# Kernel tuning notes

Measured on AMD Instinct MI355X. Metric: run time of the kernel, lower is better.

The kernel has to match this reference:

```python
import jax, jax.numpy as jnp
import numpy as np

B, N = 32, 128
V, P, L = 50000, 40, 50
WD, UD = 100, 25
D = WD + UD          # 125: LSTM hidden per direction
H2 = 2 * D           # 250: BiLSTM output
HID = 100            # hidden_dim for scorers


def setup_inputs() -> dict:
    key = jax.random.key(0)
    ks = iter(jax.random.split(key, 40))
    p = lambda shape: jax.random.normal(next(ks), shape, jnp.float32) * 0.05
    inp = {
        'word_ids': jax.random.randint(next(ks), (B, N), 0, V),
        'upos_ids': jax.random.randint(next(ks), (B, N), 0, P),
        'target_arcs': jax.random.randint(next(ks), (B, N), 0, N),
        'wlookup': p((V, WD)),
        'tlookup': p((V, UD)),  # original sizes tag table by word_count
        # LSTM layer 0 (input D=125), layer 1 (input 2D=250); f=fwd, b=bwd dir
        'l0f_Wih': p((4 * D, D)), 'l0f_Whh': p((4 * D, D)), 'l0f_b': p((4 * D,)),
        'l0b_Wih': p((4 * D, D)), 'l0b_Whh': p((4 * D, D)), 'l0b_b': p((4 * D,)),
        'l1f_Wih': p((4 * D, H2)), 'l1f_Whh': p((4 * D, D)), 'l1f_b': p((4 * D,)),
        'l1b_Wih': p((4 * D, H2)), 'l1b_Whh': p((4 * D, D)), 'l1b_b': p((4 * D,)),
        'eh_W': p((HID, H2)), 'eh_b': p((HID,)),
        'em_W': p((HID, H2)), 'em_b': p((HID,)),
        'es_W': p((1, HID)), 'es_b': p((1,)),
        'lh_W': p((HID, H2)), 'lh_b': p((HID,)),
        'lm_W': p((HID, H2)), 'lm_b': p((HID,)),
        'ls_W': p((L, HID)), 'ls_b': p((L,)),
    }
    return inp


def _lstm_dir(x, Wih, Whh, b, reverse):
    # x: [B,T,in] -> h: [B,T,H], pytorch gate order i,f,g,o
    H = Whh.shape[1]
    xg = jnp.einsum('bti,gi->btg', x, Wih) + b  # precompute input projections

    def step(carry, xt):
        h, c = carry
        g = xt + h @ Whh.T
        i, f, gg, o = jnp.split(g, 4, axis=-1)
        c = jax.nn.sigmoid(f) * c + jax.nn.sigmoid(i) * jnp.tanh(gg)
        h = jax.nn.sigmoid(o) * jnp.tanh(c)
        return (h, c), h

    h0 = jnp.zeros((x.shape[0], H), x.dtype)
    _, hs = jax.lax.scan(step, (h0, h0), jnp.swapaxes(xg, 0, 1), reverse=reverse)
    return jnp.swapaxes(hs, 0, 1)


def _bilstm(x, Wf, Uf, bf, Wb, Ub, bb):
    return jnp.concatenate([_lstm_dir(x, Wf, Uf, bf, False),
                            _lstm_dir(x, Wb, Ub, bb, True)], axis=-1)


def reference(word_ids, upos_ids, target_arcs, wlookup, tlookup,
              l0f_Wih, l0f_Whh, l0f_b, l0b_Wih, l0b_Whh, l0b_b,
              l1f_Wih, l1f_Whh, l1f_b, l1b_Wih, l1b_Whh, l1b_b,
              eh_W, eh_b, em_W, em_b, es_W, es_b,
              lh_W, lh_b, lm_W, lm_b, ls_W, ls_b):
    n = word_ids.shape[1]
    words = jnp.concatenate([wlookup[word_ids], tlookup[upos_ids]], axis=-1)  # [B,N,125]
    h0 = _bilstm(words, l0f_Wih, l0f_Whh, l0f_b, l0b_Wih, l0b_Whh, l0b_b)
    word_exprs = _bilstm(h0, l1f_Wih, l1f_Whh, l1f_b, l1b_Wih, l1b_Whh, l1b_b)  # [B,N,250]

    word_h = word_exprs @ eh_W.T + eh_b  # [B,N,100]
    word_m = word_exprs @ em_W.T + em_b
    # fused pairwise biaffine-style scoring (replaces the O(n) python loop)
    pair = jnp.tanh(word_h[:, :, None, :] + word_m[:, None, :, :])  # [B,N,N,100]
    arc_scores = jnp.einsum('bijh,h->bij', pair, es_W[0]) + es_b[0]  # [B,N,N]

    # training path: margin augmentation
    target_arcs = target_arcs.at[:, 0].set(0)
    margin = 1.0 - jax.nn.one_hot(target_arcs, n, dtype=arc_scores.dtype)
    arc_scores = arc_scores + margin

    # decode() is an external MST decoder; greedy argmax stand-in
    parsed_trees = jnp.argmax(arc_scores, axis=-1)

    tree = target_arcs  # is_train path
    rel_heads = jnp.take_along_axis(word_exprs, tree[:, :, None], axis=1)  # [B,N,250]
    rel_heads = rel_heads @ lh_W.T + lh_b
    rel_mod = word_exprs @ lm_W.T + lm_b
    rel_scores = jnp.tanh(rel_mod + rel_heads) @ ls_W.T + ls_b  # [B,N,L]
    predicted_rels = jnp.argmax(rel_scores, axis=-1)
    return (parsed_trees, predicted_rels, arc_scores, rel_scores)
```

## Files before the change

kernel.cpp:

```cpp
#include <hip/hip_runtime.h>
#include <hip/hip_bf16.h>
#include <hip/hip_fp16.h>
#include <math.h>

#define B 32
#define N 128
#define BT (B*N)
#define WD 100
#define UD 25
#define D 125
#define G4 (4*D)
#define H2 (2*D)
#define HID 100
#define L 50

__device__ __forceinline__ float fast_tanh(float x) {
    float e = __expf(2.0f * x);
    return 1.0f - 2.0f / (e + 1.0f);
}
__device__ __forceinline__ float fast_sigmoid(float x) {
    return 1.0f / (1.0f + __expf(-x));
}
__device__ __forceinline__ float bcast_lane(float v, int k) {
    return __builtin_bit_cast(float, __builtin_amdgcn_readlane(__builtin_bit_cast(int, v), k));
}
__device__ __forceinline__ unsigned bcast_lane_u(unsigned v, int k) {
    return (unsigned)__builtin_amdgcn_readlane((int)v, k);
}

__device__ __forceinline__ unsigned pack_f16x2(float lo, float hi) {
    __half hl = __float2half_rn(lo), hh = __float2half_rn(hi);
    unsigned a = (unsigned)__builtin_bit_cast(unsigned short, hl);
    unsigned b = (unsigned)__builtin_bit_cast(unsigned short, hh);
    return a | (b << 16);
}

typedef _Float16 h2_t __attribute__((ext_vector_type(2)));
__device__ __forceinline__ float dot2acc(unsigned wu, unsigned hu, float acc) {
#if __has_builtin(__builtin_amdgcn_fdot2)
    return __builtin_amdgcn_fdot2(__builtin_bit_cast(h2_t, wu),
                                  __builtin_bit_cast(h2_t, hu), acc, false);
#else
    h2_t wv = __builtin_bit_cast(h2_t, wu);
    h2_t hv = __builtin_bit_cast(h2_t, hu);
    acc = fmaf((float)wv[0], (float)hv[0], acc);
    acc = fmaf((float)wv[1], (float)hv[1], acc);
    return acc;
#endif
}

struct TJob { const float* src; float* dst; int R, C, ldo, coff, tile0, tiles_x; };
struct TArgs { TJob j[8]; };

__global__ __launch_bounds__(256)
void setup_fused(TArgs a, int n_tr,
                 const int* __restrict__ wids, const int* __restrict__ uids,
                 const float* __restrict__ wl, const float* __restrict__ tl,
                 float* __restrict__ words,
                 const float* __restrict__ l0f_b, const float* __restrict__ l0b_b,
                 const float* __restrict__ l1f_b, const float* __restrict__ l1b_b,
                 const float* __restrict__ eh_b, const float* __restrict__ em_b,
                 const float* __restrict__ lm_b,
                 float* __restrict__ b_l0, float* __restrict__ b_l1,
                 float* __restrict__ b_s3,
                 const float* __restrict__ s0, const float* __restrict__ s1,
                 const float* __restrict__ s2, const float* __restrict__ s3w,
                 unsigned* __restrict__ d0, unsigned* __restrict__ d1,
                 unsigned* __restrict__ d2, unsigned* __restrict__ d3) {
    __shared__ float tile[32][33];
    int bid = blockIdx.x;
    int tid = threadIdx.x;
    if (bid < n_tr) {
        int ji = 0;
        #pragma unroll
        for (int i = 1; i < 8; i++) if (bid >= a.j[i].tile0) ji = i;
        TJob jb = a.j[ji];
        int t = bid - jb.tile0;
        int tx = t % jb.tiles_x, ty = t / jb.tiles_x;
        int txx = tid & 31, tyy = tid >> 5;
        int k0 = tx*32, n0 = ty*32;
        #pragma unroll
        for (int dy = 0; dy < 32; dy += 8) {
            int n = n0 + tyy + dy, k = k0 + txx;
            if (n < jb.R && k < jb.C)
                tile[tyy+dy][txx] = jb.src[(size_t)n*jb.C + k];
        }
        __syncthreads();
        #pragma unroll
        for (int dy = 0; dy < 32; dy += 8) {
            int k = k0 + tyy + dy, n = n0 + txx;
            if (k < jb.C && n < jb.R)
                jb.dst[(size_t)k*jb.ldo + jb.coff + n] = tile[txx][tyy+dy];
        }
        return;
    }
    bid -= n_tr;
    if (bid < 2048) {
        int bt = bid*2 + (tid >> 7);
        int t = tid & 127;
        int wid = wids[bt], uid = uids[bt];
        if (t < WD)       words[bt*D + t] = wl[(size_t)wid*WD + t];
        else if (t < D)   words[bt*D + t] = tl[(size_t)uid*UD + (t - WD)];
        return;
    }
    bid -= 2048;
    if (bid < 9) {
        int t = bid*256 + tid;
        if (t < 500)        b_l0[t] = l0f_b[t];
        else if (t < 1000)  b_l0[t] = l0b_b[t-500];
        else if (t < 1500)  b_l1[t-1000] = l1f_b[t-1000];
        else if (t < 2000)  b_l1[t-1000] = l1b_b[t-1500];
        else if (t < 2100)  b_s3[t-2000] = eh_b[t-2000];
        else if (t < 2200)  b_s3[t-2000] = em_b[t-2100];
        else if (t < 2300)  b_s3[t-2000] = lm_b[t-2200];
        return;
    }
    bid -= 9;
    int e = bid*256 + tid;
    int m = e >> 15;
    int r = e & 32767;
    int pk = r >> 9;
    int g  = r & 511;
    const float* s = (m == 0) ? s0 : (m == 1) ? s1 : (m == 2) ? s2 : s3w;
    unsigned* dd   = (m == 0) ? d0 : (m == 1) ? d1 : (m == 2) ? d2 : d3;
    float v0 = 0.0f, v1 = 0.0f;
    if (g < 500) {
        int k0 = pk << 1;
        if (k0 < 125)     v0 = s[(size_t)g*125 + k0];
        if (k0 + 1 < 125) v1 = s[(size_t)g*125 + k0 + 1];
    }
    dd[(pk << 9) + g] = pack_f16x2(v0, v1);
}

#define MT 16
template<int CPT, int BD>
__device__ __forceinline__
void proj_body(const float* __restrict__ x, const float* __restrict__ WT,
               const float* __restrict__ bias, float* __restrict__ out,
               int Ncols, int K, int ldx, const int* __restrict__ gather_idx,
               int blk, float* xs) {
    int m0 = blk * MT;
    for (int e = threadIdx.x; e < MT * K; e += BD) {
        int r = e / K, k = e - r * K;
        int m = m0 + r;
        int row = m;
        if (gather_idx) {
            int bb = m >> 7, np = m & 127;
            row = (bb << 7) + (np == 0 ? 0 : gather_idx[m]);
        }
        xs[k*17 + r] = x[(size_t)row*ldx + k];
    }
    __syncthreads();
    int n0 = threadIdx.x;
    int lane = threadIdx.x & 63;
    float acc[CPT][MT];
    int ncl[CPT];
    #pragma unroll
    for (int j = 0; j < CPT; j++) {
        int n = n0 + j*BD;
        ncl[j] = (n < Ncols) ? n : (Ncols - 1);
        #pragma unroll
        for (int r = 0; r < MT; r++) acc[j][r] = 0.0f;
    }
    float wkc[4][CPT];
    #pragma unroll
    for (int q = 0; q < 4; q++)
        #pragma unroll
        for (int j = 0; j < CPT; j++)
            wkc[q][j] = WT[(size_t)q*Ncols + ncl[j]];
    int k0 = 0;
    for (; k0 + 8 <= K; k0 += 4) {
        float xv = xs[(k0 + (lane >> 4))*17 + (lane & 15)];
        float wkn[4][CPT];
        #pragma unroll
        for (int q = 0; q < 4; q++)
            #pragma unroll
            for (int j = 0; j < CPT; j++)
                wkn[q][j] = WT[(size_t)(k0 + 4 + q)*Ncols + ncl[j]];
        #pragma unroll
        for (int q = 0; q < 4; q++) {
            #pragma unroll
            for (int r = 0; r < 16; r++) {
                float hv = bcast_lane(xv, q*16 + r);
                #pragma unroll
                for (int j = 0; j < CPT; j++)
                    acc[j][r] = fmaf(wkc[q][j], hv, acc[j][r]);
            }
        }
        #pragma unroll
        for (int q = 0; q < 4; q++)
            #pragma unroll
            for (int j = 0; j < CPT; j++)
                wkc[q][j] = wkn[q][j];
    }
    {
        float xv = xs[(k0 + (lane >> 4))*17 + (lane & 15)];
        #pragma unroll
        for (int q = 0; q < 4; q++) {
            #pragma unroll
            for (int r = 0; r < 16; r++) {
                float hv = bcast_lane(xv, q*16 + r);
                #pragma unroll
                for (int j = 0; j < CPT; j++)
                    acc[j][r] = fmaf(wkc[q][j], hv, acc[j][r]);
            }
        }
        k0 += 4;
    }
    for (; k0 < K; k0++) {
        float xv = xs[k0*17 + (lane & 15)];
        float wk[CPT];
        #pragma unroll
        for (int j = 0; j < CPT; j++) wk[j] = WT[(size_t)k0*Ncols + ncl[j]];
        #pragma unroll
        for (int r = 0; r < 16; r++) {
            float hv = bcast_lane(xv, r);
            #pragma unroll
            for (int j = 0; j < CPT; j++)
                acc[j][r] = fmaf(wk[j], hv, acc[j][r]);
        }
    }
    #pragma unroll
    for (int j = 0; j < CPT; j++) {
        int n = n0 + j*BD;
        if (n < Ncols) {
            float bb = bias[n];
            #pragma unroll
            for (int r = 0; r < MT; r++) out[(size_t)(m0 + r)*Ncols + n] = acc[j][r] + bb;
        }
    }
}

__global__ __launch_bounds__(512)
void proj_t(const float* __restrict__ x, const float* __restrict__ WT,
            const float* __restrict__ bias, float* __restrict__ out,
            int Ncols, int K, int ldx) {
    __shared__ float xs[250 * 17 + 16];
    proj_body<2, 512>(x, WT, bias, out, Ncols, K, ldx, nullptr, blockIdx.x, xs);
}

__global__ __launch_bounds__(256)
void proj_s3lh(const float* __restrict__ x,
               const float* __restrict__ WTa, const float* __restrict__ ba,
               float* __restrict__ outa,
               const float* __restrict__ WTb, const float* __restrict__ bb,
               float* __restrict__ outb, const int* __restrict__ gather_idx) {
    __shared__ float xs[250 * 17 + 16];
    int job = blockIdx.x >> 8;
    int blk = blockIdx.x & 255;
    if (job == 0)
        proj_body<2, 256>(x, WTa, ba, outa, 300, H2, H2, nullptr, blk, xs);
    else
        proj_body<2, 256>(x, WTb, bb, outb, 100, H2, H2, gather_idx, blk, xs);
}

__global__ __launch_bounds__(512, 2)
void lstm_scan(const float* __restrict__ xgc,
               const unsigned* __restrict__ WhHf, const unsigned* __restrict__ WhHb,
               float* __restrict__ out) {
    int dir = blockIdx.x & 1;
    int b = blockIdx.x >> 1;
    const unsigned* WhH = dir ? WhHb : WhHf;
    int off = dir ? D : 0;
    int t = threadIdx.x;
    int lane = t & 63;
    int w = t >> 6;
    int ks = w >> 1;
    int cg = ((w & 1) << 6) + lane;
    int c0 = cg << 2;

    __shared__ __align__(16) float hbuf[128];
    __shared__ __align__(16) float pbuf[4*512];

    const unsigned* wp = WhH + (size_t)(ks*16)*512 + c0;

    const float* xb = xgc + (size_t)b * N * 1000 + dir * 500;
    bool xa = (ks == 0) && (cg < 125);
    float4 zero4 = make_float4(0.f, 0.f, 0.f, 0.f);
    float4 xA = zero4, xB = zero4;
    if (xa) {
        xA = *(const float4*)&xb[(size_t)(dir ? (N-1) : 0)*1000 + c0];
        xB = *(const float4*)&xb[(size_t)(dir ? (N-2) : 1)*1000 + c0];
    }

    if (t < 128) hbuf[t] = 0.0f;
    __syncthreads();

    float c = 0.0f;
    for (int ti = 0; ti < N; ti++) {
        int tt = dir ? (N-1-ti) : ti;
        uint4 wq[16];
        #pragma unroll
        for (int p = 0; p < 16; p++)
            wq[p] = *(const uint4*)&wp[(size_t)p*512];
        float2 h2 = *(const float2*)&hbuf[ks*32 + ((lane & 15) << 1)];
        unsigned vhp = pack_f16x2(h2.x, h2.y);
        float4 x_cur = xA;
        float4 xC = zero4;
        if (xa && ti + 2 < N) {
            int tn = dir ? (tt-2) : (tt+2);
            xC = *(const float4*)&xb[(size_t)tn*1000 + c0];
        }
        float a0 = x_cur.x, a1 = x_cur.y, a2 = x_cur.z, a3 = x_cur.w;
        #pragma unroll
        for (int p = 0; p < 16; p++) {
            unsigned hp = bcast_lane_u(vhp, p);
            a0 = dot2acc(wq[p].x, hp, a0);
            a1 = dot2acc(wq[p].y, hp, a1);
            a2 = dot2acc(wq[p].z, hp, a2);
            a3 = dot2acc(wq[p].w, hp, a3);
        }
        xA = xB; xB = xC;
        *(float4*)&pbuf[ks*512 + c0] = make_float4(a0, a1, a2, a3);
        asm volatile("s_waitcnt lgkmcnt(0)" ::: "memory");
        __builtin_amdgcn_s_barrier();
        asm volatile("" ::: "memory");
        if (t < D) {
            float iv = pbuf[t]       + pbuf[512+t]       + pbuf[1024+t]       + pbuf[1536+t];
            float fv = pbuf[125+t]   + pbuf[512+125+t]   + pbuf[1024+125+t]   + pbuf[1536+125+t];
            float gv = pbuf[250+t]   + pbuf[512+250+t]   + pbuf[1024+250+t]   + pbuf[1536+250+t];
            float ov = pbuf[375+t]   + pbuf[512+375+t]   + pbuf[1024+375+t]   + pbuf[1536+375+t];
            float si = fast_sigmoid(iv);
            float sf = fast_sigmoid(fv);
            float so = fast_sigmoid(ov);
            c = sf * c + si * fast_tanh(gv);
            float h = so * fast_tanh(c);
            hbuf[t] = h;
            out[(size_t)(b*N + tt)*H2 + off + t] = h;
        }
        asm volatile("s_waitcnt lgkmcnt(0)" ::: "memory");
        __builtin_amdgcn_s_barrier();
        asm volatile("" ::: "memory");
    }
}

#define ITILE 4
__global__ __launch_bounds__(128)
void arc_rel(const float* __restrict__ s3,
             const float* __restrict__ esW, const float* __restrict__ esb,
             const int* __restrict__ ta, const float* __restrict__ rh,
             const float* __restrict__ lsW, const float* __restrict__ lsb,
             float* __restrict__ arc_out, float* __restrict__ tree_out,
             float* __restrict__ rel_out, float* __restrict__ pred_out) {
    __shared__ float wms[128 * 101];
    __shared__ float whs[ITILE][HID];
    __shared__ float es[HID];
    __shared__ float sv[128];
    __shared__ int   si[128];
    int j = threadIdx.x;

    if (blockIdx.x < 1024) {
        int blk = blockIdx.x;
        int b = blk >> 5, it = blk & 31;
        for (int e = j; e < 128 * HID; e += 128) {
            int r = e / HID, h = e - r * HID;
            wms[r*101 + h] = s3[(size_t)(b*N + r)*300 + 100 + h];
        }
        for (int e = j; e < ITILE * HID; e += 128) {
            int ii = e / HID, h = e - ii * HID;
            whs[ii][h] = s3[(size_t)(b*N + it*ITILE + ii)*300 + h];
        }
        if (j < HID) es[j] = esW[j];
        __syncthreads();
        float eb = esb[0];
        const float* wmr = &wms[j * 101];
        for (int ii = 0; ii < ITILE; ii++) {
            int i = it * ITILE + ii;
            int bi = b * N + i;
            float acc = 0.0f;
            for (int h = 0; h < HID; h++)
                acc = fmaf(es[h], fast_tanh(whs[ii][h] + wmr[h]), acc);
            int tai = (i == 0) ? 0 : ta[bi];
            float score = acc + eb + 1.0f - ((j == tai) ? 1.0f : 0.0f);
            arc_out[(size_t)bi*N + j] = score;
            sv[j] = score; si[j] = j;
            __syncthreads();
            for (int s = 64; s; s >>= 1) {
                if (j < s) {
                    float ov = sv[j+s]; int oi = si[j+s];
                    if (ov > sv[j] || (ov == sv[j] && oi < si[j])) { sv[j] = ov; si[j] = oi; }
                }
                __syncthreads();
            }
            if (j == 0) tree_out[bi] = (float)si[0];
            __syncthreads();
        }
    } else {
        int bt = blockIdx.x - 1024;
        float* tv = es;
        if (j < HID)
            tv[j] = fast_tanh(s3[(size_t)bt*300 + 200 + j] + rh[(size_t)bt*HID + j]);
        __syncthreads();
        float score = -1e30f;
        if (j < L) {
            float acc = 0.0f;
            const float* wrow = lsW + j*HID;
            for (int h = 0; h < HID; h++) acc = fmaf(wrow[h], tv[h], acc);
            score = acc + lsb[j];
            rel_out[(size_t)bt*L + j] = score;
        }
        sv[j] = score; si[j] = j;
        __syncthreads();
        for (int s = 64; s; s >>= 1) {
            if (j < s) {
                float ov = sv[j+s]; int oi = si[j+s];
                if (ov > sv[j] || (ov == sv[j] && oi < si[j])) { sv[j] = ov; si[j] = oi; }
            }
            __syncthreads();
        }
        if (j == 0) pred_out[bt] = (float)si[0];
    }
}

extern "C" void kernel_launch(void* const* d_in, const int* in_sizes, int n_in,
                              void* d_out, int out_size, void* d_ws, size_t ws_size,
                              hipStream_t stream) {
    const int*   word_ids    = (const int*)  d_in[0];
    const int*   upos_ids    = (const int*)  d_in[1];
    const int*   target_arcs = (const int*)  d_in[2];
    const float* wlookup     = (const float*)d_in[3];
    const float* tlookup     = (const float*)d_in[4];
    const float* l0f_Wih = (const float*)d_in[5];
    const float* l0f_Whh = (const float*)d_in[6];
    const float* l0f_b   = (const float*)d_in[7];
    const float* l0b_Wih = (const float*)d_in[8];
    const float* l0b_Whh = (const float*)d_in[9];
    const float* l0b_b   = (const float*)d_in[10];
    const float* l1f_Wih = (const float*)d_in[11];
    const float* l1f_Whh = (const float*)d_in[12];
    const float* l1f_b   = (const float*)d_in[13];
    const float* l1b_Wih = (const float*)d_in[14];
    const float* l1b_Whh = (const float*)d_in[15];
    const float* l1b_b   = (const float*)d_in[16];
    const float* eh_W = (const float*)d_in[17];
    const float* eh_b = (const float*)d_in[18];
    const float* em_W = (const float*)d_in[19];
    const float* em_b = (const float*)d_in[20];
    const float* es_W = (const float*)d_in[21];
    const float* es_b = (const float*)d_in[22];
    const float* lh_W = (const float*)d_in[23];
    const float* lh_b = (const float*)d_in[24];
    const float* lm_W = (const float*)d_in[25];
    const float* lm_b = (const float*)d_in[26];
    const float* ls_W = (const float*)d_in[27];
    const float* ls_b = (const float*)d_in[28];

    float* out = (float*)d_out;
    float* trees_out = out;
    float* preds_out = out + BT;
    float* arc_out   = out + 2*BT;
    float* rel_out   = out + 2*BT + BT*N;

    float* ws = (float*)d_ws;
    float* A       = ws;
    float* words   = ws + 4096000;
    float* C       = ws + 4608000;
    float* WT_l0   = ws + 5632000;
    float* WT_l1   = ws + 5757000;
    float* WT_s3   = ws + 6007000;
    float* WT_lh   = ws + 6082000;
    unsigned* WhH_l0f = (unsigned*)(ws + 6107000);
    unsigned* WhH_l0b = (unsigned*)(ws + 6139768);
    unsigned* WhH_l1f = (unsigned*)(ws + 6172536);
    unsigned* WhH_l1b = (unsigned*)(ws + 6205304);
    float* b_l0    = ws + 6238072;
    float* b_l1    = ws + 6239072;
    float* b_s3    = ws + 6240072;
    float* rel_head = ws + 6241072;

    TArgs ta{};
    int n_tr = 0;
    {
        auto tiles = [](int R, int C_) { return ((C_+31)/32) * ((R+31)/32); };
        struct { const float* s; float* d; int R, C, ldo, coff; } js[8] = {
            { l0f_Wih, WT_l0, 500, 125, 1000, 0 },
            { l0b_Wih, WT_l0, 500, 125, 1000, 500 },
            { l1f_Wih, WT_l1, 500, 250, 1000, 0 },
            { l1b_Wih, WT_l1, 500, 250, 1000, 500 },
            { eh_W, WT_s3, 100, 250, 300, 0 },
            { em_W, WT_s3, 100, 250, 300, 100 },
            { lm_W, WT_s3, 100, 250, 300, 200 },
            { lh_W, WT_lh, 100, 250, 100, 0 },
        };
        for (int i = 0; i < 8; i++) {
            ta.j[i].src = js[i].s;  ta.j[i].dst = js[i].d;
            ta.j[i].R = js[i].R;    ta.j[i].C = js[i].C;
            ta.j[i].ldo = js[i].ldo; ta.j[i].coff = js[i].coff;
            ta.j[i].tile0 = n_tr;
            ta.j[i].tiles_x = (js[i].C + 31) / 32;
            n_tr += tiles(js[i].R, js[i].C);
        }
    }
    setup_fused<<<n_tr + 2048 + 9 + 512, 256, 0, stream>>>(
        ta, n_tr, word_ids, upos_ids, wlookup, tlookup, words,
        l0f_b, l0b_b, l1f_b, l1b_b, eh_b, em_b, lm_b,
        b_l0, b_l1, b_s3,
        l0f_Whh, l0b_Whh, l1f_Whh, l1b_Whh,
        WhH_l0f, WhH_l0b, WhH_l1f, WhH_l1b);

    proj_t<<<BT/MT, 512, 0, stream>>>(words, WT_l0, b_l0, A, 1000, D, D);

    lstm_scan<<<B*2, 512, 0, stream>>>(A, WhH_l0f, WhH_l0b, C);

    proj_t<<<BT/MT, 512, 0, stream>>>(C, WT_l1, b_l1, A, 1000, H2, H2);

    lstm_scan<<<B*2, 512, 0, stream>>>(A, WhH_l1f, WhH_l1b, C);

    proj_s3lh<<<512, 256, 0, stream>>>(C, WT_s3, b_s3, A,
                                       WT_lh, lh_b, rel_head, target_arcs);

    arc_rel<<<1024 + BT, 128, 0, stream>>>(A, es_W, es_b, target_arcs, rel_head,
                                           ls_W, ls_b, arc_out, trees_out,
                                           rel_out, preds_out);
}
```

Measured before the change: 534.2 us.

## Stage recurrent weights in LDS and compute gate updates redundantly per wave

The LSTM scan kernel now copies its fp16-packed recurrent weight slice into a large dynamic LDS buffer once, instead of reloading it from global memory every timestep. Each wave recomputes the cell update for its own 32 hidden units and forms the packed h operand through a lane shuffle, which removes the shared hbuf and the second barrier per step. The partial-sum buffer is double-buffered to keep this safe with a single barrier. This trades a large LDS footprint (144 KB, one block per CU) and redundant activation math for lower per-step latency on the serial recurrence.

New measurement: 606.7 us. 13.6% more time.

```diff
diff --git a/kernel.cpp b/kernel.cpp
--- a/kernel.cpp
+++ b/kernel.cpp
@@ -254,10 +254,13 @@
         proj_body<2, 256>(x, WTb, bb, outb, 100, H2, H2, gather_idx, blk, xs);
 }
 
-__global__ __launch_bounds__(512, 2)
+__global__ __launch_bounds__(512)
 void lstm_scan(const float* __restrict__ xgc,
                const unsigned* __restrict__ WhHf, const unsigned* __restrict__ WhHb,
                float* __restrict__ out) {
+    extern __shared__ float smem[];
+    unsigned* wlds = (unsigned*)smem;
+    float* pbuf = smem + 32768;
     int dir = blockIdx.x & 1;
     int b = blockIdx.x >> 1;
     const unsigned* WhH = dir ? WhHb : WhHf;
@@ -269,10 +272,15 @@
     int cg = ((w & 1) << 6) + lane;
     int c0 = cg << 2;
 
-    __shared__ __align__(16) float hbuf[128];
-    __shared__ __align__(16) float pbuf[4*512];
-
-    const unsigned* wp = WhH + (size_t)(ks*16)*512 + c0;
+    {
+        const unsigned* wpg = WhH + (size_t)(ks*16)*512 + c0;
+        #pragma unroll
+        for (int p = 0; p < 16; p++) {
+            uint4 u = *(const uint4*)&wpg[(size_t)p*512];
+            *(uint4*)&wlds[((p << 9) + t) << 2] = u;
+        }
+    }
+    __syncthreads();
 
     const float* xb = xgc + (size_t)b * N * 1000 + dir * 500;
     bool xa = (ks == 0) && (cg < 125);
@@ -283,18 +291,19 @@
         xB = *(const float4*)&xb[(size_t)(dir ? (N-2) : 1)*1000 + c0];
     }
 
-    if (t < 128) hbuf[t] = 0.0f;
-    __syncthreads();
-
-    float c = 0.0f;
+    int t4 = ks*32 + (lane & 31);
+    bool act = (lane < 32) && (t4 < 125);
+    bool sto = act && ((w & 1) == 0);
+
+    unsigned vhp = 0;
+    float c = 0.0f, h = 0.0f;
+
     for (int ti = 0; ti < N; ti++) {
         int tt = dir ? (N-1-ti) : ti;
         uint4 wq[16];
         #pragma unroll
         for (int p = 0; p < 16; p++)
-            wq[p] = *(const uint4*)&wp[(size_t)p*512];
-        float2 h2 = *(const float2*)&hbuf[ks*32 + ((lane & 15) << 1)];
-        unsigned vhp = pack_f16x2(h2.x, h2.y);
+            wq[p] = *(const uint4*)&wlds[((p << 9) + t) << 2];
         float4 x_cur = xA;
         float4 xC = zero4;
         if (xa && ti + 2 < N) {
@@ -304,33 +313,33 @@
         float a0 = x_cur.x, a1 = x_cur.y, a2 = x_cur.z, a3 = x_cur.w;
         #pragma unroll
         for (int p = 0; p < 16; p++) {
-            unsigned hp = bcast_lane_u(vhp, p);
+            unsigned hp = bcast_lane_u(vhp, 2*p);
             a0 = dot2acc(wq[p].x, hp, a0);
             a1 = dot2acc(wq[p].y, hp, a1);
             a2 = dot2acc(wq[p].z, hp, a2);
             a3 = dot2acc(wq[p].w, hp, a3);
         }
         xA = xB; xB = xC;
-        *(float4*)&pbuf[ks*512 + c0] = make_float4(a0, a1, a2, a3);
+        float* pb = &pbuf[(ti & 1) << 11];
+        *(float4*)&pb[ks*512 + c0] = make_float4(a0, a1, a2, a3);
         asm volatile("s_waitcnt lgkmcnt(0)" ::: "memory");
         __builtin_amdgcn_s_barrier();
         asm volatile("" ::: "memory");
-        if (t < D) {
-            float iv = pbuf[t]       + pbuf[512+t]       + pbuf[1024+t]       + pbuf[1536+t];
-            float fv = pbuf[125+t]   + pbuf[512+125+t]   + pbuf[1024+125+t]   + pbuf[1536+125+t];
-            float gv = pbuf[250+t]   + pbuf[512+250+t]   + pbuf[1024+250+t]   + pbuf[1536+250+t];
-            float ov = pbuf[375+t]   + pbuf[512+375+t]   + pbuf[1024+375+t]   + pbuf[1536+375+t];
+        if (act) {
+            float iv = pb[t4]       + pb[512+t4]       + pb[1024+t4]       + pb[1536+t4];
+            float fv = pb[125+t4]   + pb[512+125+t4]   + pb[1024+125+t4]   + pb[1536+125+t4];
+            float gv = pb[250+t4]   + pb[512+250+t4]   + pb[1024+250+t4]   + pb[1536+250+t4];
+            float ov = pb[375+t4]   + pb[512+375+t4]   + pb[1024+375+t4]   + pb[1536+375+t4];
             float si = fast_sigmoid(iv);
             float sf = fast_sigmoid(fv);
             float so = fast_sigmoid(ov);
             c = sf * c + si * fast_tanh(gv);
-            float h = so * fast_tanh(c);
-            hbuf[t] = h;
-            out[(size_t)(b*N + tt)*H2 + off + t] = h;
-        }
-        asm volatile("s_waitcnt lgkmcnt(0)" ::: "memory");
-        __builtin_amdgcn_s_barrier();
-        asm volatile("" ::: "memory");
+            h = so * fast_tanh(c);
+            if (sto)
+                out[(size_t)(b*N + tt)*H2 + off + t4] = h;
+        }
+        float hn = __shfl_xor(h, 1);
+        vhp = pack_f16x2(h, hn);
     }
 }
 
@@ -468,6 +477,14 @@
     float* b_s3    = ws + 6240072;
     float* rel_head = ws + 6241072;
 
+    static bool attr_done = false;
+    if (!attr_done) {
+        (void)hipFuncSetAttribute(reinterpret_cast<const void*>(lstm_scan),
+                                  hipFuncAttributeMaxDynamicSharedMemorySize,
+                                  147456);
+        attr_done = true;
+    }
+
     TArgs ta{};
     int n_tr = 0;
     {
@@ -500,11 +517,11 @@
 
     proj_t<<<BT/MT, 512, 0, stream>>>(words, WT_l0, b_l0, A, 1000, D, D);
 
-    lstm_scan<<<B*2, 512, 0, stream>>>(A, WhH_l0f, WhH_l0b, C);
+    lstm_scan<<<B*2, 512, 147456, stream>>>(A, WhH_l0f, WhH_l0b, C);
 
     proj_t<<<BT/MT, 512, 0, stream>>>(C, WT_l1, b_l1, A, 1000, H2, H2);
 
-    lstm_scan<<<B*2, 512, 0, stream>>>(A, WhH_l1f, WhH_l1b, C);
+    lstm_scan<<<B*2, 512, 147456, stream>>>(A, WhH_l1f, WhH_l1b, C);
 
     proj_s3lh<<<512, 256, 0, stream>>>(C, WT_s3, b_s3, A,
                                        WT_lh, lh_b, rel_head, target_arcs);
```
